# Performance work log

Measured on AMD Instinct MI355X. Metric: run time of the kernel, lower is better.

Reference implementation:

```python
import jax, jax.numpy as jnp
import numpy as np

NUM_CLASSES = 80
NUM_MASKED = 3
SCALE_XY = 1.2
STRIDE = 8.0
# yolov4 anchors for mask [0,1,2], divided by stride
_ANCHORS = np.array([[12.0, 16.0], [19.0, 36.0], [40.0, 28.0]], dtype=np.float32) / STRIDE


def setup_inputs() -> dict:
    key = jax.random.key(0)
    x = jax.random.normal(key, (16, NUM_MASKED * (5 + NUM_CLASSES), 76, 76), dtype=jnp.float32)
    return {"x": x}


def reference(x):
    B, C, H, W = x.shape
    A, nc, s = NUM_MASKED, NUM_CLASSES, SCALE_XY
    anchors = jnp.asarray(_ANCHORS)  # [A, 2]
    o = x.reshape(B, A, 5 + nc, H, W)
    # yolov4 (new_coords==0) transforms
    bxy = jax.nn.sigmoid(o[:, :, 0:2]) * s - 0.5 * (s - 1.0)  # [B,A,2,H,W]
    bwh = jnp.exp(o[:, :, 2:4])                               # [B,A,2,H,W]
    det = jax.nn.sigmoid(o[:, :, 4])                          # [B,A,H,W]
    cls = jax.nn.sigmoid(o[:, :, 5:])                         # [B,A,nc,H,W]
    grid_x = jnp.arange(W, dtype=x.dtype)                     # broadcasts over W
    grid_y = jnp.arange(H, dtype=x.dtype)[:, None]            # broadcasts over H
    bx = (bxy[:, :, 0] + grid_x) / W
    by = (bxy[:, :, 1] + grid_y) / H
    bw = bwh[:, :, 0] * anchors[None, :, 0, None, None] / W
    bh = bwh[:, :, 1] * anchors[None, :, 1, None, None] / H
    bx1 = bx - bw * 0.5
    by1 = by - bh * 0.5
    bx2 = bx - bw * 0.5 + bw
    by2 = by - bh * 0.5 + bh
    boxes = jnp.stack((bx1, by1, bx2, by2), axis=-1).reshape(B, A * H * W, 4)
    # cls [B,A,nc,H,W] -> [B,A,H,W,nc], scaled by objectness
    confs = (cls * det[:, :, None]).transpose(0, 1, 3, 4, 2).reshape(B, A * H * W, nc)
    return jnp.concatenate([boxes, confs], axis=-1)  # [B, A*H*W, 4+nc]
```

## Files before the change

### kernel.cpp

```cpp
#include <hip/hip_runtime.h>
#include <hip/hip_bf16.h>


#define YHW 5776
#define PT 112
#define NT 52
#define LSTRIDE 113
#define NTHREADS 512

typedef float f4v __attribute__((ext_vector_type(4)));

__device__ __forceinline__ float fsigmoid(float v) {
    return __builtin_amdgcn_rcpf(1.0f + __expf(-v));
}

template<int QN>
__device__ __forceinline__ void build(const float* __restrict__ src,
                                      float (*lds)[LSTRIDE], int tid) {
    constexpr int NQ = 85 * QN;
    constexpr int NJ = (NQ + NTHREADS - 1) / NTHREADS;
    f4v r[NJ];
    #pragma unroll
    for (int j = 0; j < NJ; ++j) {
        const int idx = tid + NTHREADS * j;
        if (idx < NQ) {
            const int ch = idx / QN;
            const int q  = idx - ch * QN;
            r[j] = *reinterpret_cast<const f4v*>(src + (size_t)ch * YHW + 4 * q);
        }
    }
    #pragma unroll
    for (int j = 0; j < NJ; ++j) {
        const int idx = tid + NTHREADS * j;
        if (idx < NQ) {
            const int ch = idx / QN;
            const int q  = idx - ch * QN;
            f4v v = r[j];
            int row;
            if (ch < 2) {
                v.x = fsigmoid(v.x) * 1.2f - 0.1f;
                v.y = fsigmoid(v.y) * 1.2f - 0.1f;
                v.z = fsigmoid(v.z) * 1.2f - 0.1f;
                v.w = fsigmoid(v.w) * 1.2f - 0.1f;
                row = ch;
            } else if (ch < 4) {
                v.x = __expf(v.x); v.y = __expf(v.y);
                v.z = __expf(v.z); v.w = __expf(v.w);
                row = ch;
            } else {
                v.x = fsigmoid(v.x); v.y = fsigmoid(v.y);
                v.z = fsigmoid(v.z); v.w = fsigmoid(v.w);
                row = (ch == 4) ? 84 : ch - 1;
            }
            const int p4 = 4 * q;
            lds[row][p4 + 0] = v.x;
            lds[row][p4 + 1] = v.y;
            lds[row][p4 + 2] = v.z;
            lds[row][p4 + 3] = v.w;
        }
    }
}

__global__ __launch_bounds__(NTHREADS) void yolo_kernel(const float* __restrict__ x,
                                                        float* __restrict__ out) {
    const int blk  = blockIdx.x;
    const int tile = blk % NT;
    const int ba   = blk / NT;
    const int a    = ba % 3;
    const int p0   = tile * PT;
    const int npos = (tile == NT - 1) ? 64 : PT;

    __shared__ float lds[85][LSTRIDE];

    const float* __restrict__ src = x + (size_t)ba * 85 * YHW + p0;
    const int tid = threadIdx.x;

    if (npos == PT) build<28>(src, lds, tid);
    else            build<16>(src, lds, tid);
    __syncthreads();

    const float ax  = (a == 0) ? 1.5f : ((a == 1) ? 2.375f : 5.0f);
    const float ay  = (a == 0) ? 2.0f : ((a == 1) ? 4.5f : 3.5f);
    const float inv = 1.0f / 76.0f;
    float* __restrict__ dst = out + ((size_t)ba * YHW + p0) * 84;

    const int total = npos * 21;
    for (int u = tid; u < total; u += NTHREADS) {
        const int pp = u / 21;
        const int c  = u - 21 * pp;
        f4v o;
        if (c == 0) {
            const float sx = lds[0][pp];
            const float sy = lds[1][pp];
            const float ew = lds[2][pp];
            const float eh = lds[3][pp];
            const int p = p0 + pp;
            const int h = p / 76;
            const int w = p - 76 * h;
            const float bxc = (sx + (float)w) * inv;
            const float byc = (sy + (float)h) * inv;
            const float bw  = ew * ax * inv;
            const float bh  = eh * ay * inv;
            const float bx1 = bxc - 0.5f * bw;
            const float by1 = byc - 0.5f * bh;
            o.x = bx1; o.y = by1; o.z = bx1 + bw; o.w = by1 + bh;
        } else {
            const float det = lds[84][pp];
            o.x = lds[4 * c + 0][pp] * det;
            o.y = lds[4 * c + 1][pp] * det;
            o.z = lds[4 * c + 2][pp] * det;
            o.w = lds[4 * c + 3][pp] * det;
        }
        *reinterpret_cast<f4v*>(dst + (size_t)pp * 84 + 4 * c) = o;
    }
}

extern "C" void kernel_launch(void* const* d_in, const int* in_sizes, int n_in,
                              void* d_out, int out_size, void* d_ws, size_t ws_size,
                              hipStream_t stream) {
    const float* x = (const float*)d_in[0];
    float* out = (float*)d_out;
    const int nblocks = 48 * NT;
    yolo_kernel<<<nblocks, NTHREADS, 0, stream>>>(x, out);
}
```

Baseline: 35.63 us.

## Process four image rows per block with register double-buffered prefetch

```diff
diff --git a/kernel.cpp b/kernel.cpp
--- a/kernel.cpp
+++ b/kernel.cpp
@@ -1,12 +1,15 @@
 #include <hip/hip_runtime.h>
-#include <hip/hip_bf16.h>
 
 
 #define YHW 5776
-#define PT 112
-#define NT 52
-#define LSTRIDE 113
+#define W76 76
+#define NROWS 4
+#define NRB 19
+#define LSTRIDE 77
 #define NTHREADS 512
+#define QN 19
+#define NQ (85 * QN)
+#define NJ 4
 
 typedef float f4v __attribute__((ext_vector_type(4)));
 
@@ -14,21 +17,20 @@
     return __builtin_amdgcn_rcpf(1.0f + __expf(-v));
 }
 
-template<int QN>
-__device__ __forceinline__ void build(const float* __restrict__ src,
-                                      float (*lds)[LSTRIDE], int tid) {
-    constexpr int NQ = 85 * QN;
-    constexpr int NJ = (NQ + NTHREADS - 1) / NTHREADS;
-    f4v r[NJ];
+__device__ __forceinline__ void issue_loads(const float* __restrict__ src, int toff,
+                                            f4v r[NJ], int tid) {
     #pragma unroll
     for (int j = 0; j < NJ; ++j) {
         const int idx = tid + NTHREADS * j;
         if (idx < NQ) {
             const int ch = idx / QN;
             const int q  = idx - ch * QN;
-            r[j] = *reinterpret_cast<const f4v*>(src + (size_t)ch * YHW + 4 * q);
+            r[j] = *reinterpret_cast<const f4v*>(src + (size_t)ch * YHW + 4 * q + toff);
         }
     }
+}
+
+__device__ __forceinline__ void transform(const f4v r[NJ], float (*lds)[LSTRIDE], int tid) {
     #pragma unroll
     for (int j = 0; j < NJ; ++j) {
         const int idx = tid + NTHREADS * j;
@@ -61,58 +63,73 @@
     }
 }
 
+__device__ __forceinline__ void drain(const float (*lds)[LSTRIDE], float* __restrict__ dst,
+                                      int h, float ax, float ay, int tid) {
+    const float inv = 1.0f / 76.0f;
+    constexpr int total = W76 * 21;
+    #pragma unroll
+    for (int u0 = 0; u0 < total; u0 += NTHREADS) {
+        const int u = u0 + tid;
+        if (u < total) {
+            const int pp = u / 21;
+            const int c  = u - 21 * pp;
+            f4v o;
+            if (c == 0) {
+                const float sx = lds[0][pp];
+                const float sy = lds[1][pp];
+                const float ew = lds[2][pp];
+                const float eh = lds[3][pp];
+                const float bxc = (sx + (float)pp) * inv;
+                const float byc = (sy + (float)h) * inv;
+                const float bw  = ew * ax * inv;
+                const float bh  = eh * ay * inv;
+                const float bx1 = bxc - 0.5f * bw;
+                const float by1 = byc - 0.5f * bh;
+                o.x = bx1; o.y = by1; o.z = bx1 + bw; o.w = by1 + bh;
+            } else {
+                const float det = lds[84][pp];
+                o.x = lds[4 * c + 0][pp] * det;
+                o.y = lds[4 * c + 1][pp] * det;
+                o.z = lds[4 * c + 2][pp] * det;
+                o.w = lds[4 * c + 3][pp] * det;
+            }
+            *reinterpret_cast<f4v*>(dst + (size_t)pp * 84 + 4 * c) = o;
+        }
+    }
+}
+
 __global__ __launch_bounds__(NTHREADS) void yolo_kernel(const float* __restrict__ x,
                                                         float* __restrict__ out) {
     const int blk  = blockIdx.x;
-    const int tile = blk % NT;
-    const int ba   = blk / NT;
+    const int rb   = blk % NRB;
+    const int ba   = blk / NRB;
     const int a    = ba % 3;
-    const int p0   = tile * PT;
-    const int npos = (tile == NT - 1) ? 64 : PT;
+    const int row0 = rb * NROWS;
 
     __shared__ float lds[85][LSTRIDE];
 
-    const float* __restrict__ src = x + (size_t)ba * 85 * YHW + p0;
     const int tid = threadIdx.x;
+    const float* __restrict__ srcbase = x + (size_t)ba * 85 * YHW + (size_t)row0 * W76;
+    float* __restrict__ dstbase = out + ((size_t)ba * YHW + (size_t)row0 * W76) * 84;
 
-    if (npos == PT) build<28>(src, lds, tid);
-    else            build<16>(src, lds, tid);
-    __syncthreads();
+    const float ax = (a == 0) ? 1.5f : ((a == 1) ? 2.375f : 5.0f);
+    const float ay = (a == 0) ? 2.0f : ((a == 1) ? 4.5f : 3.5f);
 
-    const float ax  = (a == 0) ? 1.5f : ((a == 1) ? 2.375f : 5.0f);
-    const float ay  = (a == 0) ? 2.0f : ((a == 1) ? 4.5f : 3.5f);
-    const float inv = 1.0f / 76.0f;
-    float* __restrict__ dst = out + ((size_t)ba * YHW + p0) * 84;
+    f4v rA[NJ], rB[NJ];
+    issue_loads(srcbase, 0, rA, tid);
 
-    const int total = npos * 21;
-    for (int u = tid; u < total; u += NTHREADS) {
-        const int pp = u / 21;
-        const int c  = u - 21 * pp;
-        f4v o;
-        if (c == 0) {
-            const float sx = lds[0][pp];
-            const float sy = lds[1][pp];
-            const float ew = lds[2][pp];
-            const float eh = lds[3][pp];
-            const int p = p0 + pp;
-            const int h = p / 76;
-            const int w = p - 76 * h;
-            const float bxc = (sx + (float)w) * inv;
-            const float byc = (sy + (float)h) * inv;
-            const float bw  = ew * ax * inv;
-            const float bh  = eh * ay * inv;
-            const float bx1 = bxc - 0.5f * bw;
-            const float by1 = byc - 0.5f * bh;
-            o.x = bx1; o.y = by1; o.z = bx1 + bw; o.w = by1 + bh;
-        } else {
-            const float det = lds[84][pp];
-            o.x = lds[4 * c + 0][pp] * det;
-            o.y = lds[4 * c + 1][pp] * det;
-            o.z = lds[4 * c + 2][pp] * det;
-            o.w = lds[4 * c + 3][pp] * det;
-        }
-        *reinterpret_cast<f4v*>(dst + (size_t)pp * 84 + 4 * c) = o;
-    }
+#define STEP(T, CUR, NXT, ISLAST)                                              \
+    transform(CUR, lds, tid);                                                  \
+    __syncthreads();                                                           \
+    if (!(ISLAST)) issue_loads(srcbase, ((T) + 1) * W76, NXT, tid);            \
+    drain(lds, dstbase + (size_t)(T) * W76 * 84, row0 + (T), ax, ay, tid);     \
+    if (!(ISLAST)) __syncthreads();
+
+    STEP(0, rA, rB, 0)
+    STEP(1, rB, rA, 0)
+    STEP(2, rA, rB, 0)
+    STEP(3, rB, rA, 1)
+#undef STEP
 }
 
 extern "C" void kernel_launch(void* const* d_in, const int* in_sizes, int n_in,
@@ -120,6 +137,6 @@
                               hipStream_t stream) {
     const float* x = (const float*)d_in[0];
     float* out = (float*)d_out;
-    const int nblocks = 48 * NT;
+    const int nblocks = 48 * NRB;
     yolo_kernel<<<nblocks, NTHREADS, 0, stream>>>(x, out);
 }
```

Measured after the change: 37.89 us. +6.3%, slower.
